# Performance work log

Hardware: AMD Instinct MI355X
Metric: run time of the kernel (lower is better)

## Reference

```python
import math
import jax, jax.numpy as jnp
import numpy as np

B, S, D = 1, 2048, 4096
H, KV, Dh = 32, 8, 128          # query heads, kv heads, head dim
G = H // KV                      # GQA group size
THETA = 10000.0
FACTOR = 4.0
BETA_FAST, BETA_SLOW, ORIG_MAX = 32, 1, 32768


def _yarn_rope_cache(seq_len):
    """YaRN-scaled RoPE cos/sin cache, matching YaRNRotaryEmbedding._build_cache."""
    inv_freq = 1.0 / (THETA ** (np.arange(0, Dh, 2, dtype=np.float32) / Dh))
    low = ORIG_MAX / (2 * math.pi * BETA_SLOW)
    high = ORIG_MAX / (2 * math.pi * BETA_FAST)
    freq = 1.0 / inv_freq
    smooth = np.clip((freq - low) / (high - low), 0.0, 1.0)
    inv_freq = (1.0 - smooth) * inv_freq + smooth * (inv_freq / FACTOR)
    t = np.arange(seq_len, dtype=np.float32)
    freqs = np.outer(t, inv_freq)                 # [S, Dh/2]
    emb = np.concatenate([freqs, freqs], axis=-1) # [S, Dh]
    return np.cos(emb).astype(np.float32), np.sin(emb).astype(np.float32)


def _rotate_half(x):
    x1, x2 = jnp.split(x, 2, axis=-1)
    return jnp.concatenate([-x2, x1], axis=-1)


def setup_inputs() -> dict:
    key = jax.random.key(0)
    k0, k1, k2, k3, k4 = jax.random.split(key, 5)
    scale = 0.02
    hidden_states = jax.random.normal(k0, (B, S, D), jnp.float32)
    Wq = jax.random.normal(k1, (H * Dh, D), jnp.float32) * scale
    Wk = jax.random.normal(k2, (KV * Dh, D), jnp.float32) * scale
    Wv = jax.random.normal(k3, (KV * Dh, D), jnp.float32) * scale
    Wo = jax.random.normal(k4, (D, H * Dh), jnp.float32) * scale
    cos_np, sin_np = _yarn_rope_cache(S)
    return {"hidden_states": hidden_states, "Wq": Wq, "Wk": Wk, "Wv": Wv,
            "Wo": Wo, "cos": jnp.asarray(cos_np), "sin": jnp.asarray(sin_np)}


def reference(hidden_states, Wq, Wk, Wv, Wo, cos, sin):
    x = hidden_states
    b, s, _ = x.shape
    # QKV projections (Linear, no bias): y = x @ W.T
    q = jnp.einsum('bsd,ed->bse', x, Wq).reshape(b, s, H, Dh).transpose(0, 2, 1, 3)   # [B,H,S,Dh]
    k = jnp.einsum('bsd,ed->bse', x, Wk).reshape(b, s, KV, Dh).transpose(0, 2, 1, 3)  # [B,KV,S,Dh]
    v = jnp.einsum('bsd,ed->bse', x, Wv).reshape(b, s, KV, Dh).transpose(0, 2, 1, 3)  # [B,KV,S,Dh]
    # YaRN RoPE (cos/sin: [S,Dh], broadcast over batch/head)
    c = cos[None, None, :, :]
    sn = sin[None, None, :, :]
    q = q * c + _rotate_half(q) * sn
    k = k * c + _rotate_half(k) * sn
    # GQA: group query heads over kv heads instead of materializing repeat_interleave
    qg = q.reshape(b, KV, G, s, Dh)
    scores = jnp.einsum('bkgqd,bknd->bkgqn', qg, k) / math.sqrt(Dh)  # [B,KV,G,S,S]
    causal = jnp.tril(jnp.ones((s, s), dtype=bool))
    scores = jnp.where(causal[None, None, None], scores, jnp.finfo(scores.dtype).min)
    w = jax.nn.softmax(scores.astype(jnp.float32), axis=-1).astype(x.dtype)
    attn = jnp.einsum('bkgqn,bknd->bkgqd', w, v)                      # [B,KV,G,S,Dh]
    attn = attn.reshape(b, H, s, Dh).transpose(0, 2, 1, 3).reshape(b, s, H * Dh)
    return jnp.einsum('bse,de->bsd', attn, Wo)
```

## Files before the change

### kernel.cpp

```cpp
#include <hip/hip_runtime.h>

#define S_LEN 2048
#define DMODEL 4096
#define NH 32
#define NKV 8
#define DH 128
#define QDIM (NH*DH)
#define NQKV 6144
#define SCALE 0.08838834764831845f

typedef __attribute__((ext_vector_type(8))) short short8;
typedef __attribute__((ext_vector_type(4))) float f32x4;
typedef __attribute__((ext_vector_type(4))) unsigned short us4;

__device__ __forceinline__ unsigned short f2bf(float f) {
  union { float f; unsigned int u; } v; v.f = f;
  unsigned int r = v.u + 0x7FFFu + ((v.u >> 16) & 1u);
  return (unsigned short)(r >> 16);
}
__device__ __forceinline__ float bf2f(unsigned short h) {
  union { unsigned int u; float f; } v; v.u = ((unsigned int)h) << 16;
  return v.f;
}
__device__ __forceinline__ short8 pack_bf16x8(float4 a, float4 b) {
  unsigned int u0, u1, u2, u3;
  asm("v_cvt_pk_bf16_f32 %0, %1, %2" : "=v"(u0) : "v"(a.x), "v"(a.y));
  asm("v_cvt_pk_bf16_f32 %0, %1, %2" : "=v"(u1) : "v"(a.z), "v"(a.w));
  asm("v_cvt_pk_bf16_f32 %0, %1, %2" : "=v"(u2) : "v"(b.x), "v"(b.y));
  asm("v_cvt_pk_bf16_f32 %0, %1, %2" : "=v"(u3) : "v"(b.z), "v"(b.w));
  union { unsigned int u[4]; short8 s; } r;
  r.u[0] = u0; r.u[1] = u1; r.u[2] = u2; r.u[3] = u3;
  return r.s;
}

__global__ __launch_bounds__(256) void cvt_x(const float* __restrict__ in,
                                             unsigned short* __restrict__ out) {
  int i = blockIdx.x * 256 + threadIdx.x;
  const float4 f = reinterpret_cast<const float4*>(in)[i];
  us4 o;
  o.x = f2bf(f.x); o.y = f2bf(f.y); o.z = f2bf(f.z); o.w = f2bf(f.w);
  reinterpret_cast<us4*>(out)[i] = o;
}

__global__ __launch_bounds__(512) void gemm8pqkv(const unsigned short* __restrict__ A,
                                                 const float* __restrict__ Wq,
                                                 const float* __restrict__ Wk,
                                                 const float* __restrict__ Wv,
                                                 unsigned short* __restrict__ Cv) {
  constexpr int K_ = 4096, N_ = 6144;
  constexpr int BM_ = 256, BN_ = 192;
  constexpr int ATILE = BM_ * 128;
  constexpr int BTILE = BN_ * 128;
  constexpr int BUF = ATILE + BTILE;
  constexpr int LPA = BM_ / 64;
  constexpr int LPB = BN_ / 64;
  constexpr int MI = 8, NF = 3;
  constexpr int MIL = 4, NFL = 1;
  constexpr int NT = K_ / 64;
  constexpr int CHN = 4;
  __shared__ char lds[2 * BUF];

  const int tid = threadIdx.x;
  const int lane = tid & 63, wave = tid >> 6;
  const int wm = wave >> 2, wn = wave & 3;
  const int fr = lane & 15, fq = lane >> 4;

  const int lin = blockIdx.x;
  const int xcd = lin & 7;
  const int slot = lin >> 3;
  const long n0 = (long)(xcd * CHN + slot % CHN) * BN_;
  const long m0 = (long)(slot / CHN) * BM_;

  const char* pB[LPB];
  int bslot[LPB];
#pragma unroll
  for (int u = 0; u < LPB; ++u) {
    int b = u * 8192 + tid * 16;
    int row = b >> 7;
    int colx = (b & 127) ^ ((row & 7) << 4);
    long n = n0 + row;
    const float* base = (n < 4096) ? Wq + n * (long)K_
                      : (n < 5120) ? Wk + (n - 4096) * (long)K_
                                   : Wv + (n - 5120) * (long)K_;
    pB[u] = (const char*)base + (long)colx * 2;
    bslot[u] = b;
  }
  float4 breg[LPB][2];

  auto B_ISSUE = [&](int t) {
#pragma unroll
    for (int u = 0; u < LPB; ++u) {
      breg[u][0] = *reinterpret_cast<const float4*>(pB[u] + (long)t * 256);
      breg[u][1] = *reinterpret_cast<const float4*>(pB[u] + (long)t * 256 + 16);
    }
  };
  auto B_WRITE = [&](int c) {
#pragma unroll
    for (int u = 0; u < LPB; ++u)
      *reinterpret_cast<short8*>(lds + c * BUF + ATILE + bslot[u]) =
          pack_bf16x8(breg[u][0], breg[u][1]);
  };
  auto STAGE_A = [&](int t, int c) {
#pragma unroll
    for (int u = 0; u < LPA; ++u) {
      int b = u * 8192 + tid * 16;
      int row = b >> 7;
      int off = (b & 127) ^ ((row & 7) << 4);
      __builtin_amdgcn_global_load_lds(
        (const __attribute__((address_space(1))) void*)((const char*)A + ((m0 + row) * (long)K_ + t * 64) * 2 + off),
        (__attribute__((address_space(3))) void*)(lds + c * BUF + b), 16, 0, 0);
    }
  };

  f32x4 acc[MI][NF] = {};
  short8 af[MI][2];
  short8 bf[NF][2];

  B_ISSUE(0);
  asm volatile("s_waitcnt vmcnt(0)" ::: "memory");
  B_WRITE(0);
  B_ISSUE(1);
  STAGE_A(0, 0); STAGE_A(1, 1);
  asm volatile("s_waitcnt vmcnt(8)" ::: "memory");
  B_WRITE(1);
  asm volatile("s_waitcnt vmcnt(0)" ::: "memory");
  asm volatile("s_waitcnt lgkmcnt(0)" ::: "memory");
  __builtin_amdgcn_s_barrier();

  for (int t = 0; t < NT; ++t) {
    const int c = t & 1;
    const char* tb = lds + c * BUF;

#pragma unroll
    for (int mi = 0; mi < MIL; ++mi) {
      int row = wm * (BM_ / 2) + mi * 16 + fr;
#pragma unroll
      for (int ks = 0; ks < 2; ++ks)
        af[mi][ks] = *(const short8*)(tb + row * 128 + ((ks * 64 + fq * 16) ^ ((row & 7) << 4)));
    }
#pragma unroll
    for (int ni = 0; ni < NFL; ++ni) {
      int row = wn * (BN_ / 4) + ni * 16 + fr;
#pragma unroll
      for (int ks = 0; ks < 2; ++ks)
        bf[ni][ks] = *(const short8*)(tb + ATILE + row * 128 + ((ks * 64 + fq * 16) ^ ((row & 7) << 4)));
    }
    asm volatile("s_waitcnt vmcnt(4)" ::: "memory");
    if (t > 0 && t + 1 < NT) B_WRITE((t + 1) & 1);
    if (t + 2 < NT) B_ISSUE(t + 2);
    __builtin_amdgcn_s_barrier();
    __builtin_amdgcn_s_setprio(1);
#pragma unroll
    for (int mi = 0; mi < MIL; ++mi)
#pragma unroll
      for (int ni = 0; ni < NFL; ++ni)
#pragma unroll
        for (int ks = 0; ks < 2; ++ks)
          acc[mi][ni] = __builtin_amdgcn_mfma_f32_16x16x32_bf16(af[mi][ks], bf[ni][ks], acc[mi][ni], 0, 0, 0);
    __builtin_amdgcn_s_setprio(0);
    __builtin_amdgcn_s_barrier();

#pragma unroll
    for (int mi = MIL; mi < MI; ++mi) {
      int row = wm * (BM_ / 2) + mi * 16 + fr;
#pragma unroll
      for (int ks = 0; ks < 2; ++ks)
        af[mi][ks] = *(const short8*)(tb + row * 128 + ((ks * 64 + fq * 16) ^ ((row & 7) << 4)));
    }
#pragma unroll
    for (int ni = NFL; ni < NF; ++ni) {
      int row = wn * (BN_ / 4) + ni * 16 + fr;
#pragma unroll
      for (int ks = 0; ks < 2; ++ks)
        bf[ni][ks] = *(const short8*)(tb + ATILE + row * 128 + ((ks * 64 + fq * 16) ^ ((row & 7) << 4)));
    }
    __builtin_amdgcn_s_barrier();
    __builtin_amdgcn_s_setprio(1);
#pragma unroll
    for (int mi = 0; mi < MIL; ++mi)
#pragma unroll
      for (int ni = NFL; ni < NF; ++ni)
#pragma unroll
        for (int ks = 0; ks < 2; ++ks)
          acc[mi][ni] = __builtin_amdgcn_mfma_f32_16x16x32_bf16(af[mi][ks], bf[ni][ks], acc[mi][ni], 0, 0, 0);
    __builtin_amdgcn_s_setprio(0);
    __builtin_amdgcn_s_barrier();

    if (t + 2 < NT) STAGE_A(t + 2, c);
    __builtin_amdgcn_s_setprio(1);
#pragma unroll
    for (int mi = MIL; mi < MI; ++mi)
#pragma unroll
      for (int ni = 0; ni < NFL; ++ni)
#pragma unroll
        for (int ks = 0; ks < 2; ++ks)
          acc[mi][ni] = __builtin_amdgcn_mfma_f32_16x16x32_bf16(af[mi][ks], bf[ni][ks], acc[mi][ni], 0, 0, 0);
    __builtin_amdgcn_s_setprio(0);
    __builtin_amdgcn_s_barrier();

    __builtin_amdgcn_s_setprio(1);
#pragma unroll
    for (int mi = MIL; mi < MI; ++mi)
#pragma unroll
      for (int ni = NFL; ni < NF; ++ni)
#pragma unroll
        for (int ks = 0; ks < 2; ++ks)
          acc[mi][ni] = __builtin_amdgcn_mfma_f32_16x16x32_bf16(af[mi][ks], bf[ni][ks], acc[mi][ni], 0, 0, 0);
    __builtin_amdgcn_s_setprio(0);
    if (t + 2 < NT) { asm volatile("s_waitcnt vmcnt(10)" ::: "memory"); }
    else if (t + 1 < NT) { asm volatile("s_waitcnt vmcnt(0)" ::: "memory"); }
    __builtin_amdgcn_s_barrier();
  }

#pragma unroll
  for (int mi = 0; mi < MI; ++mi)
#pragma unroll
    for (int ni = 0; ni < NF; ++ni)
#pragma unroll
      for (int j = 0; j < 4; ++j) {
        long r = m0 + wm * (BM_ / 2) + mi * 16 + fq * 4 + j;
        long cc = n0 + wn * (BN_ / 4) + ni * 16 + fr;
        Cv[r * N_ + cc] = f2bf(acc[mi][ni][j]);
      }
}

template<int M_, int N_, int K_, int BM_, int BN_, int OUT_BF16, int CHN>
__global__ __launch_bounds__(512) void gemm8p(const unsigned short* __restrict__ A,
                                              const unsigned short* __restrict__ B,
                                              void* __restrict__ Cv) {
  constexpr int ATILE = BM_ * 128;
  constexpr int BTILE = BN_ * 128;
  constexpr int BUF = ATILE + BTILE;
  constexpr int LPA = BM_ / 64;
  constexpr int LPB = BN_ / 64;
  constexpr int VM  = LPA + LPB;
  constexpr int MI = BM_ / 32, NF = BN_ / 64;
  constexpr int MIL = MI / 2, NFL = NF / 2;
  constexpr int NT = K_ / 64;
  __shared__ char lds[2 * BUF];

  const int tid = threadIdx.x;
  const int lane = tid & 63, wave = tid >> 6;
  const int wm = wave >> 2, wn = wave & 3;
  const int fr = lane & 15, fq = lane >> 4;

  const int lin = blockIdx.x;
  const int xcd = lin & 7;
  const int slot = lin >> 3;
  const long n0 = (long)(xcd * CHN + slot % CHN) * BN_;
  const long m0 = (long)(slot / CHN) * BM_;

  auto STAGE_A = [&](int t, int c) {
#pragma unroll
    for (int u = 0; u < LPA; ++u) {
      int b = u * 8192 + tid * 16;
      int row = b >> 7;
      int off = (b & 127) ^ ((row & 7) << 4);
      __builtin_amdgcn_global_load_lds(
        (const __attribute__((address_space(1))) void*)((const char*)A + ((m0 + row) * (long)K_ + t * 64) * 2 + off),
        (__attribute__((address_space(3))) void*)(lds + c * BUF + b), 16, 0, 0);
    }
  };
  auto STAGE_B = [&](int t, int c) {
#pragma unroll
    for (int u = 0; u < LPB; ++u) {
      int b = u * 8192 + tid * 16;
      int row = b >> 7;
      int off = (b & 127) ^ ((row & 7) << 4);
      __builtin_amdgcn_global_load_lds(
        (const __attribute__((address_space(1))) void*)((const char*)B + ((n0 + row) * (long)K_ + t * 64) * 2 + off),
        (__attribute__((address_space(3))) void*)(lds + c * BUF + ATILE + b), 16, 0, 0);
    }
  };
#define VMCNT_STEADY() do { if constexpr (VM == 6) asm volatile("s_waitcnt vmcnt(6)" ::: "memory"); \
                            else if constexpr (VM == 7) asm volatile("s_waitcnt vmcnt(7)" ::: "memory"); \
                            else asm volatile("s_waitcnt vmcnt(8)" ::: "memory"); } while (0)

  f32x4 acc[MI][NF] = {};
  short8 af[MI][2];
  short8 bf[NF][2];

  STAGE_A(0, 0); STAGE_B(0, 0);
  STAGE_A(1, 1); STAGE_B(1, 1);
  VMCNT_STEADY();
  __builtin_amdgcn_s_barrier();

  for (int t = 0; t < NT; ++t) {
    const int c = t & 1;
    const char* tb = lds + c * BUF;

#pragma unroll
    for (int mi = 0; mi < MIL; ++mi) {
      int row = wm * (BM_ / 2) + mi * 16 + fr;
#pragma unroll
      for (int ks = 0; ks < 2; ++ks)
        af[mi][ks] = *(const short8*)(tb + row * 128 + ((ks * 64 + fq * 16) ^ ((row & 7) << 4)));
    }
#pragma unroll
    for (int ni = 0; ni < NFL; ++ni) {
      int row = wn * (BN_ / 4) + ni * 16 + fr;
#pragma unroll
      for (int ks = 0; ks < 2; ++ks)
        bf[ni][ks] = *(const short8*)(tb + ATILE + row * 128 + ((ks * 64 + fq * 16) ^ ((row & 7) << 4)));
    }
    __builtin_amdgcn_s_barrier();
    __builtin_amdgcn_s_setprio(1);
#pragma unroll
    for (int mi = 0; mi < MIL; ++mi)
#pragma unroll
      for (int ni = 0; ni < NFL; ++ni)
#pragma unroll
        for (int ks = 0; ks < 2; ++ks)
          acc[mi][ni] = __builtin_amdgcn_mfma_f32_16x16x32_bf16(af[mi][ks], bf[ni][ks], acc[mi][ni], 0, 0, 0);
    __builtin_amdgcn_s_setprio(0);
    __builtin_amdgcn_s_barrier();

#pragma unroll
    for (int mi = MIL; mi < MI; ++mi) {
      int row = wm * (BM_ / 2) + mi * 16 + fr;
#pragma unroll
      for (int ks = 0; ks < 2; ++ks)
        af[mi][ks] = *(const short8*)(tb + row * 128 + ((ks * 64 + fq * 16) ^ ((row & 7) << 4)));
    }
#pragma unroll
    for (int ni = NFL; ni < NF; ++ni) {
      int row = wn * (BN_ / 4) + ni * 16 + fr;
#pragma unroll
      for (int ks = 0; ks < 2; ++ks)
        bf[ni][ks] = *(const short8*)(tb + ATILE + row * 128 + ((ks * 64 + fq * 16) ^ ((row & 7) << 4)));
    }
    __builtin_amdgcn_s_barrier();
    __builtin_amdgcn_s_setprio(1);
#pragma unroll
    for (int mi = 0; mi < MIL; ++mi)
#pragma unroll
      for (int ni = NFL; ni < NF; ++ni)
#pragma unroll
        for (int ks = 0; ks < 2; ++ks)
          acc[mi][ni] = __builtin_amdgcn_mfma_f32_16x16x32_bf16(af[mi][ks], bf[ni][ks], acc[mi][ni], 0, 0, 0);
    __builtin_amdgcn_s_setprio(0);
    __builtin_amdgcn_s_barrier();

    if (t + 2 < NT) STAGE_A(t + 2, c);
    __builtin_amdgcn_s_setprio(1);
#pragma unroll
    for (int mi = MIL; mi < MI; ++mi)
#pragma unroll
      for (int ni = 0; ni < NFL; ++ni)
#pragma unroll
        for (int ks = 0; ks < 2; ++ks)
          acc[mi][ni] = __builtin_amdgcn_mfma_f32_16x16x32_bf16(af[mi][ks], bf[ni][ks], acc[mi][ni], 0, 0, 0);
    __builtin_amdgcn_s_setprio(0);
    __builtin_amdgcn_s_barrier();

    if (t + 2 < NT) STAGE_B(t + 2, c);
    __builtin_amdgcn_s_setprio(1);
#pragma unroll
    for (int mi = MIL; mi < MI; ++mi)
#pragma unroll
      for (int ni = NFL; ni < NF; ++ni)
#pragma unroll
        for (int ks = 0; ks < 2; ++ks)
          acc[mi][ni] = __builtin_amdgcn_mfma_f32_16x16x32_bf16(af[mi][ks], bf[ni][ks], acc[mi][ni], 0, 0, 0);
    __builtin_amdgcn_s_setprio(0);
    if (t + 2 < NT) { VMCNT_STEADY(); }
    else if (t + 1 < NT) { asm volatile("s_waitcnt vmcnt(0)" ::: "memory"); }
    __builtin_amdgcn_s_barrier();
  }
#undef VMCNT_STEADY

#pragma unroll
  for (int mi = 0; mi < MI; ++mi)
#pragma unroll
    for (int ni = 0; ni < NF; ++ni)
#pragma unroll
      for (int j = 0; j < 4; ++j) {
        long r = m0 + wm * (BM_ / 2) + mi * 16 + fq * 4 + j;
        long cc = n0 + wn * (BN_ / 4) + ni * 16 + fr;
        float v = acc[mi][ni][j];
        if (OUT_BF16) ((unsigned short*)Cv)[r * N_ + cc] = f2bf(v);
        else          ((float*)Cv)[r * N_ + cc] = v;
      }
}

__global__ __launch_bounds__(256) void ropek_tv(unsigned short* __restrict__ C,
                                                const float* __restrict__ cosb,
                                                const float* __restrict__ sinb,
                                                unsigned short* __restrict__ VT) {
  __shared__ unsigned short tbuf[64][72];
  const int blk = blockIdx.x;
  if (blk < 4096) {
    int idx = blk * 256 + threadIdx.x;
    int i = idx & 63;
    int t = idx >> 6;
    int hh = t & 7;
    int s = t >> 3;
    unsigned short* row = C + (size_t)s * NQKV + 4096 + hh * DH;
    float c  = cosb[s * DH + i];
    float sn = sinb[s * DH + i];
    float x1 = bf2f(row[i]);
    float x2 = bf2f(row[i + 64]);
    row[i]      = f2bf(x1 * c - x2 * sn);
    row[i + 64] = f2bf(x2 * c + x1 * sn);
    return;
  }
  const int b2 = blk - 4096;
  const unsigned short* Vbuf = C + 5120;
  const int s0 = (b2 & 31) * 64, e0 = (b2 >> 5) * 64;
  const int r = threadIdx.x >> 3, c = (threadIdx.x & 7) * 8;
#pragma unroll
  for (int half = 0; half < 2; ++half) {
    int row = r + half * 32;
    *reinterpret_cast<short8*>(&tbuf[row][c]) =
        *reinterpret_cast<const short8*>(Vbuf + (size_t)(s0 + row) * NQKV + e0 + c);
  }
  __syncthreads();
  const int hh = e0 >> 7, dbase = e0 & 127;
#pragma unroll
  for (int half = 0; half < 2; ++half) {
    int row = r + half * 32;
    short8 o;
#pragma unroll
    for (int j = 0; j < 8; ++j) ((unsigned short*)&o)[j] = tbuf[c + j][row];
    *reinterpret_cast<short8*>(VT + (size_t)hh * (DH * (size_t)S_LEN)
                               + (size_t)(dbase + row) * S_LEN + s0 + c) = o;
  }
}

__global__ __launch_bounds__(256) void attn_fwd(const unsigned short* __restrict__ C,
                                                const unsigned short* __restrict__ VT,
                                                unsigned short* __restrict__ Ob,
                                                const float* __restrict__ Wo,
                                                unsigned short* __restrict__ Wob,
                                                const float* __restrict__ cosb,
                                                const float* __restrict__ sinb) {
  __shared__ unsigned short KVs[2][8192];
  __shared__ unsigned short Pl[4][16 * 40];
  const int tid = threadIdx.x, lane = tid & 63, wave = tid >> 6;
  const int kvh = blockIdx.x & 7;
  const int p = blockIdx.x >> 3;
  const int h = kvh * 4 + wave;
  const int fr = lane & 15, fq = lane >> 4;
  const int q0s[2] = { p * 16, (127 - p) * 16 };
  const int tilesA = (p * 16 + 47) >> 5;
  const int tilesB = ((127 - p) * 16 + 47) >> 5;

  const unsigned short* Qbase = C + (size_t)h * DH;
  const unsigned short* Kbase = C + 4096 + (size_t)kvh * DH;
  const unsigned short* Vbase = VT + (size_t)kvh * (DH * (size_t)S_LEN);

  const int wq0 = blockIdx.x * 8192 + tid;
  float4 wreg;

  short8 qf[2][4];
#pragma unroll
  for (int s = 0; s < 2; ++s)
#pragma unroll
    for (int dc = 0; dc < 4; ++dc)
      qf[s][dc] = *reinterpret_cast<const short8*>(
          Qbase + (size_t)(q0s[s] + fr) * NQKV + dc * 32 + fq * 8);

#pragma unroll
  for (int s = 0; s < 2; ++s) {
    const int row = q0s[s] + fr;
#pragma unroll
    for (int dc = 0; dc < 2; ++dc)
#pragma unroll
      for (int e = 0; e < 8; ++e) {
        int d = dc * 32 + fq * 8 + e;
        float cs = cosb[row * DH + d];
        float sn = sinb[row * DH + d];
        float x1 = bf2f((unsigned short)qf[s][dc][e]);
        float x2 = bf2f((unsigned short)qf[s][dc + 2][e]);
        qf[s][dc][e]     = (short)f2bf((x1 * cs - x2 * sn) * SCALE);
        qf[s][dc + 2][e] = (short)f2bf((x2 * cs + x1 * sn) * SCALE);
      }
  }

  f32x4 o_acc[2][8] = {};
  float mrow[2][4] = {{-1e30f,-1e30f,-1e30f,-1e30f},{-1e30f,-1e30f,-1e30f,-1e30f}};
  float lpart[2][4] = {};

  auto STAGE = [&](int t, int buf) {
    const int kv0 = t * 32;
    char* dst = (char*)&KVs[buf][0];
#pragma unroll
    for (int sh = 0; sh < 2; ++sh) {
      int b = sh * 4096 + tid * 16;
      int krow = b >> 8;
      int kcol = (b & 255) ^ ((krow & 7) << 4);
      __builtin_amdgcn_global_load_lds(
          (const __attribute__((address_space(1))) void*)(Kbase + (size_t)(kv0 + krow) * NQKV + (kcol >> 1)),
          (__attribute__((address_space(3))) void*)(dst + b), 16, 0, 0);
      int vrow = b >> 6;
      int vcol = (b & 63) ^ ((((vrow ^ (vrow >> 2)) & 3)) << 4);
      __builtin_amdgcn_global_load_lds(
          (const __attribute__((address_space(1))) void*)(Vbase + (size_t)vrow * S_LEN + kv0 + (vcol >> 1)),
          (__attribute__((address_space(3))) void*)(dst + 8192 + b), 16, 0, 0);
    }
  };

  int cur = 0;
  STAGE(0, 0);
  asm volatile("s_waitcnt vmcnt(0)" ::: "memory");
  __syncthreads();

  for (int t = 0; t < tilesB; ++t) {
    const int kv0 = t * 32;

    if (t > 0 && t <= 32) {
      us4 o;
      o.x = f2bf(wreg.x); o.y = f2bf(wreg.y); o.z = f2bf(wreg.z); o.w = f2bf(wreg.w);
      reinterpret_cast<us4*>(Wob)[wq0 + (t - 1) * 256] = o;
    }
    if (t < 32) wreg = reinterpret_cast<const float4*>(Wo)[wq0 + t * 256];

    if (t + 1 < tilesB) STAGE(t + 1, cur ^ 1);
    const char* kvb = (const char*)&KVs[cur][0];

#pragma unroll
    for (int s = 0; s < 2; ++s) {
      if (s == 0 && t >= tilesA) continue;
      const int q0 = q0s[s];

      f32x4 sacc[2] = {};
#pragma unroll
      for (int nt = 0; nt < 2; ++nt) {
        const int row = nt * 16 + fr;
#pragma unroll
        for (int dc = 0; dc < 4; ++dc) {
          short8 kf = *reinterpret_cast<const short8*>(
              kvb + row * 256 + ((dc * 64 + fq * 16) ^ ((row & 7) << 4)));
          sacc[nt] = __builtin_amdgcn_mfma_f32_16x16x32_bf16(qf[s][dc], kf, sacc[nt], 0, 0, 0);
        }
      }

      const bool needMask = (kv0 + 32 > q0);
      if (needMask) {
#pragma unroll
        for (int j = 0; j < 4; ++j) {
          int qrow = q0 + fq * 4 + j;
#pragma unroll
          for (int nt = 0; nt < 2; ++nt)
            sacc[nt][j] = ((kv0 + nt*16 + fr) <= qrow) ? sacc[nt][j] : -1e30f;
        }
      }
      bool ok = true;
      float lm[4];
#pragma unroll
      for (int j = 0; j < 4; ++j) {
        lm[j] = fmaxf(sacc[0][j], sacc[1][j]);
        ok = ok && (lm[j] <= mrow[s][j] + 8.f);
      }
      if (!__all(ok)) {
#pragma unroll
        for (int j = 0; j < 4; ++j) {
          float rm = lm[j];
          rm = fmaxf(rm, __shfl_xor(rm, 1));
          rm = fmaxf(rm, __shfl_xor(rm, 2));
          rm = fmaxf(rm, __shfl_xor(rm, 4));
          rm = fmaxf(rm, __shfl_xor(rm, 8));
          float mnew = fmaxf(mrow[s][j], rm);
          float corr = __expf(mrow[s][j] - mnew);
          mrow[s][j] = mnew;
          lpart[s][j] *= corr;
#pragma unroll
          for (int dt = 0; dt < 8; ++dt) o_acc[s][dt][j] *= corr;
        }
      }
#pragma unroll
      for (int j = 0; j < 4; ++j) {
        float p0 = __expf(sacc[0][j] - mrow[s][j]);
        float p1 = __expf(sacc[1][j] - mrow[s][j]);
        lpart[s][j] += p0 + p1;
        unsigned int u;
        asm("v_cvt_pk_bf16_f32 %0, %1, %2" : "=v"(u) : "v"(p0), "v"(p1));
        Pl[wave][(fq*4 + j)*40 + fr]      = (unsigned short)u;
        Pl[wave][(fq*4 + j)*40 + 16 + fr] = (unsigned short)(u >> 16);
      }
      asm volatile("s_waitcnt lgkmcnt(0)" ::: "memory");
      __builtin_amdgcn_sched_barrier(0);

      short8 pa = *reinterpret_cast<const short8*>(&Pl[wave][fr*40 + fq*8]);
#pragma unroll
      for (int dt = 0; dt < 8; ++dt) {
        const int row = dt * 16 + fr;
        short8 bv = *reinterpret_cast<const short8*>(
            kvb + 8192 + row * 64 + ((fq * 16) ^ ((((row ^ (row >> 2)) & 3)) << 4)));
        o_acc[s][dt] = __builtin_amdgcn_mfma_f32_16x16x32_bf16(pa, bv, o_acc[s][dt], 0, 0, 0);
      }
    }

    asm volatile("s_waitcnt vmcnt(0)" ::: "memory");
    __syncthreads();
    cur ^= 1;
  }

#pragma unroll
  for (int s = 0; s < 2; ++s)
#pragma unroll
    for (int j = 0; j < 4; ++j) {
      float l = lpart[s][j];
      l += __shfl_xor(l, 1);
      l += __shfl_xor(l, 2);
      l += __shfl_xor(l, 4);
      l += __shfl_xor(l, 8);
      float inv = 1.f / l;
      size_t r = (size_t)q0s[s] + fq*4 + j;
#pragma unroll
      for (int dt = 0; dt < 8; ++dt)
        Ob[r * QDIM + h * DH + dt*16 + fr] = f2bf(o_acc[s][dt][j] * inv);
    }
}

extern "C" void kernel_launch(void* const* d_in, const int* in_sizes, int n_in,
                              void* d_out, int out_size, void* d_ws, size_t ws_size,
                              hipStream_t stream) {
  (void)in_sizes; (void)n_in; (void)out_size; (void)ws_size;
  const float* x    = (const float*)d_in[0];
  const float* Wq   = (const float*)d_in[1];
  const float* Wk   = (const float*)d_in[2];
  const float* Wv   = (const float*)d_in[3];
  const float* Wo   = (const float*)d_in[4];
  const float* cosb = (const float*)d_in[5];
  const float* sinb = (const float*)d_in[6];

  char* ws = (char*)d_ws;
  unsigned short* xb    = (unsigned short*)(ws);
  unsigned short* Wob   = (unsigned short*)(ws + 67108864);
  unsigned short* Cqkv  = (unsigned short*)(ws + 100663296);
  unsigned short* VT    = (unsigned short*)(ws + 125829120);
  unsigned short* Ab    = xb;

  cvt_x<<<8192, 256, 0, stream>>>(x, xb);

  gemm8pqkv<<<256, 512, 0, stream>>>(xb, Wq, Wk, Wv, Cqkv);

  ropek_tv<<<4608, 256, 0, stream>>>(Cqkv, cosb, sinb, VT);

  attn_fwd<<<512, 256, 0, stream>>>(Cqkv, VT, Ab, Wo, Wob, cosb, sinb);

  gemm8p<2048, 4096, 4096, 128, 256, 0, 2><<<256, 512, 0, stream>>>(Ab, Wob, d_out);
}
```

Measured before the change: 285.3 us.

## Double-buffer weight prefetch registers and unroll QKV GEMM K-loop by two

Splits the fp32 weight prefetch registers into two alternating sets and unrolls the K-loop by two, so each tile's global loads go into the set not currently waiting to be converted. The bf16 conversion and LDS write of the next B tile move later in the iteration, after the A-stage issue, with retuned vmcnt waits. The aim is to hide weight-load latency behind more MFMA work. The cost is more VGPRs, which could hurt occupancy or cause spills. The first-quadrant MFMA code is also hard-coded to a single B fragment, which assumes NFL is 1.

```diff
diff --git a/kernel.cpp b/kernel.cpp
--- a/kernel.cpp
+++ b/kernel.cpp
@@ -85,21 +85,21 @@
     pB[u] = (const char*)base + (long)colx * 2;
     bslot[u] = b;
   }
-  float4 breg[LPB][2];
-
-  auto B_ISSUE = [&](int t) {
-#pragma unroll
-    for (int u = 0; u < LPB; ++u) {
-      breg[u][0] = *reinterpret_cast<const float4*>(pB[u] + (long)t * 256);
-      breg[u][1] = *reinterpret_cast<const float4*>(pB[u] + (long)t * 256 + 16);
-    }
-  };
-  auto B_WRITE = [&](int c) {
-#pragma unroll
-    for (int u = 0; u < LPB; ++u)
-      *reinterpret_cast<short8*>(lds + c * BUF + ATILE + bslot[u]) =
-          pack_bf16x8(breg[u][0], breg[u][1]);
-  };
+  float4 bregs0[LPB][2], bregs1[LPB][2];
+
+#define B_ISSUE(T, REGS) do { \
+  _Pragma("unroll") \
+  for (int u = 0; u < LPB; ++u) { \
+    REGS[u][0] = *reinterpret_cast<const float4*>(pB[u] + (long)(T) * 256); \
+    REGS[u][1] = *reinterpret_cast<const float4*>(pB[u] + (long)(T) * 256 + 16); \
+  } } while (0)
+#define B_WRITE(C, REGS) do { \
+  _Pragma("unroll") \
+  for (int u = 0; u < LPB; ++u) \
+    *reinterpret_cast<short8*>(lds + (C) * BUF + ATILE + bslot[u]) = \
+        pack_bf16x8(REGS[u][0], REGS[u][1]); \
+  } while (0)
+
   auto STAGE_A = [&](int t, int c) {
 #pragma unroll
     for (int u = 0; u < LPA; ++u) {
@@ -116,101 +116,105 @@
   short8 af[MI][2];
   short8 bf[NF][2];
 
-  B_ISSUE(0);
+  B_ISSUE(0, bregs0);
   asm volatile("s_waitcnt vmcnt(0)" ::: "memory");
-  B_WRITE(0);
-  B_ISSUE(1);
+  B_WRITE(0, bregs0);
+  B_ISSUE(1, bregs1);
   STAGE_A(0, 0); STAGE_A(1, 1);
-  asm volatile("s_waitcnt vmcnt(8)" ::: "memory");
-  B_WRITE(1);
-  asm volatile("s_waitcnt vmcnt(0)" ::: "memory");
+  asm volatile("s_waitcnt vmcnt(4)" ::: "memory");
   asm volatile("s_waitcnt lgkmcnt(0)" ::: "memory");
   __builtin_amdgcn_s_barrier();
 
-  for (int t = 0; t < NT; ++t) {
-    const int c = t & 1;
-    const char* tb = lds + c * BUF;
-
-#pragma unroll
-    for (int mi = 0; mi < MIL; ++mi) {
-      int row = wm * (BM_ / 2) + mi * 16 + fr;
-#pragma unroll
-      for (int ks = 0; ks < 2; ++ks)
-        af[mi][ks] = *(const short8*)(tb + row * 128 + ((ks * 64 + fq * 16) ^ ((row & 7) << 4)));
-    }
-#pragma unroll
-    for (int ni = 0; ni < NFL; ++ni) {
-      int row = wn * (BN_ / 4) + ni * 16 + fr;
-#pragma unroll
-      for (int ks = 0; ks < 2; ++ks)
-        bf[ni][ks] = *(const short8*)(tb + ATILE + row * 128 + ((ks * 64 + fq * 16) ^ ((row & 7) << 4)));
-    }
-    asm volatile("s_waitcnt vmcnt(4)" ::: "memory");
-    if (t > 0 && t + 1 < NT) B_WRITE((t + 1) & 1);
-    if (t + 2 < NT) B_ISSUE(t + 2);
-    __builtin_amdgcn_s_barrier();
-    __builtin_amdgcn_s_setprio(1);
-#pragma unroll
-    for (int mi = 0; mi < MIL; ++mi)
-#pragma unroll
-      for (int ni = 0; ni < NFL; ++ni)
-#pragma unroll
-        for (int ks = 0; ks < 2; ++ks)
-          acc[mi][ni] = __builtin_amdgcn_mfma_f32_16x16x32_bf16(af[mi][ks], bf[ni][ks], acc[mi][ni], 0, 0, 0);
-    __builtin_amdgcn_s_setprio(0);
-    __builtin_amdgcn_s_barrier();
-
-#pragma unroll
-    for (int mi = MIL; mi < MI; ++mi) {
-      int row = wm * (BM_ / 2) + mi * 16 + fr;
-#pragma unroll
-      for (int ks = 0; ks < 2; ++ks)
-        af[mi][ks] = *(const short8*)(tb + row * 128 + ((ks * 64 + fq * 16) ^ ((row & 7) << 4)));
-    }
-#pragma unroll
-    for (int ni = NFL; ni < NF; ++ni) {
-      int row = wn * (BN_ / 4) + ni * 16 + fr;
-#pragma unroll
-      for (int ks = 0; ks < 2; ++ks)
-        bf[ni][ks] = *(const short8*)(tb + ATILE + row * 128 + ((ks * 64 + fq * 16) ^ ((row & 7) << 4)));
-    }
-    __builtin_amdgcn_s_barrier();
-    __builtin_amdgcn_s_setprio(1);
-#pragma unroll
-    for (int mi = 0; mi < MIL; ++mi)
-#pragma unroll
-      for (int ni = NFL; ni < NF; ++ni)
-#pragma unroll
-        for (int ks = 0; ks < 2; ++ks)
-          acc[mi][ni] = __builtin_amdgcn_mfma_f32_16x16x32_bf16(af[mi][ks], bf[ni][ks], acc[mi][ni], 0, 0, 0);
-    __builtin_amdgcn_s_setprio(0);
-    __builtin_amdgcn_s_barrier();
-
-    if (t + 2 < NT) STAGE_A(t + 2, c);
-    __builtin_amdgcn_s_setprio(1);
-#pragma unroll
-    for (int mi = MIL; mi < MI; ++mi)
-#pragma unroll
-      for (int ni = 0; ni < NFL; ++ni)
-#pragma unroll
-        for (int ks = 0; ks < 2; ++ks)
-          acc[mi][ni] = __builtin_amdgcn_mfma_f32_16x16x32_bf16(af[mi][ks], bf[ni][ks], acc[mi][ni], 0, 0, 0);
-    __builtin_amdgcn_s_setprio(0);
-    __builtin_amdgcn_s_barrier();
-
-    __builtin_amdgcn_s_setprio(1);
-#pragma unroll
-    for (int mi = MIL; mi < MI; ++mi)
-#pragma unroll
-      for (int ni = NFL; ni < NF; ++ni)
-#pragma unroll
-        for (int ks = 0; ks < 2; ++ks)
-          acc[mi][ni] = __builtin_amdgcn_mfma_f32_16x16x32_bf16(af[mi][ks], bf[ni][ks], acc[mi][ni], 0, 0, 0);
-    __builtin_amdgcn_s_setprio(0);
-    if (t + 2 < NT) { asm volatile("s_waitcnt vmcnt(10)" ::: "memory"); }
-    else if (t + 1 < NT) { asm volatile("s_waitcnt vmcnt(0)" ::: "memory"); }
-    __builtin_amdgcn_s_barrier();
-  }
+#define KTILE(T, C, REGS_CUR, REGS_OTH) do { \
+  const int t_ = (T); \
+  const char* tb = lds + (C) * BUF; \
+   \
+  _Pragma("unroll") \
+  for (int mi = 0; mi < MIL; ++mi) { \
+    int row = wm * (BM_ / 2) + mi * 16 + fr; \
+    _Pragma("unroll") \
+    for (int ks = 0; ks < 2; ++ks) \
+      af[mi][ks] = *(const short8*)(tb + row * 128 + ((ks * 64 + fq * 16) ^ ((row & 7) << 4))); \
+  } \
+  { int row = wn * (BN_ / 4) + fr; \
+    _Pragma("unroll") \
+    for (int ks = 0; ks < 2; ++ks) \
+      bf[0][ks] = *(const short8*)(tb + ATILE + row * 128 + ((ks * 64 + fq * 16) ^ ((row & 7) << 4))); } \
+  if (t_ + 2 < NT) B_ISSUE(t_ + 2, REGS_CUR); \
+  __builtin_amdgcn_s_barrier(); \
+  __builtin_amdgcn_s_setprio(1); \
+  _Pragma("unroll") \
+  for (int mi = 0; mi < MIL; ++mi) \
+    _Pragma("unroll") \
+    for (int ks = 0; ks < 2; ++ks) \
+      acc[mi][0] = __builtin_amdgcn_mfma_f32_16x16x32_bf16(af[mi][ks], bf[0][ks], acc[mi][0], 0, 0, 0); \
+  __builtin_amdgcn_s_setprio(0); \
+  __builtin_amdgcn_s_barrier(); \
+   \
+  _Pragma("unroll") \
+  for (int mi = MIL; mi < MI; ++mi) { \
+    int row = wm * (BM_ / 2) + mi * 16 + fr; \
+    _Pragma("unroll") \
+    for (int ks = 0; ks < 2; ++ks) \
+      af[mi][ks] = *(const short8*)(tb + row * 128 + ((ks * 64 + fq * 16) ^ ((row & 7) << 4))); \
+  } \
+  _Pragma("unroll") \
+  for (int ni = NFL; ni < NF; ++ni) { \
+    int row = wn * (BN_ / 4) + ni * 16 + fr; \
+    _Pragma("unroll") \
+    for (int ks = 0; ks < 2; ++ks) \
+      bf[ni][ks] = *(const short8*)(tb + ATILE + row * 128 + ((ks * 64 + fq * 16) ^ ((row & 7) << 4))); \
+  } \
+  __builtin_amdgcn_s_barrier(); \
+  __builtin_amdgcn_s_setprio(1); \
+  _Pragma("unroll") \
+  for (int mi = 0; mi < MIL; ++mi) \
+    _Pragma("unroll") \
+    for (int ni = NFL; ni < NF; ++ni) \
+      _Pragma("unroll") \
+      for (int ks = 0; ks < 2; ++ks) \
+        acc[mi][ni] = __builtin_amdgcn_mfma_f32_16x16x32_bf16(af[mi][ks], bf[ni][ks], acc[mi][ni], 0, 0, 0); \
+  __builtin_amdgcn_s_setprio(0); \
+  __builtin_amdgcn_s_barrier(); \
+   \
+  if (t_ + 2 < NT) { \
+    STAGE_A(t_ + 2, (C)); \
+    asm volatile("s_waitcnt vmcnt(14)" ::: "memory"); \
+  } else { \
+    asm volatile("s_waitcnt vmcnt(0)" ::: "memory"); \
+  } \
+  if (t_ + 1 < NT) B_WRITE((C) ^ 1, REGS_OTH); \
+  __builtin_amdgcn_s_setprio(1); \
+  _Pragma("unroll") \
+  for (int mi = MIL; mi < MI; ++mi) \
+    _Pragma("unroll") \
+    for (int ks = 0; ks < 2; ++ks) \
+      acc[mi][0] = __builtin_amdgcn_mfma_f32_16x16x32_bf16(af[mi][ks], bf[0][ks], acc[mi][0], 0, 0, 0); \
+  __builtin_amdgcn_s_setprio(0); \
+  __builtin_amdgcn_s_barrier(); \
+   \
+  __builtin_amdgcn_s_setprio(1); \
+  _Pragma("unroll") \
+  for (int mi = MIL; mi < MI; ++mi) \
+    _Pragma("unroll") \
+    for (int ni = NFL; ni < NF; ++ni) \
+      _Pragma("unroll") \
+      for (int ks = 0; ks < 2; ++ks) \
+        acc[mi][ni] = __builtin_amdgcn_mfma_f32_16x16x32_bf16(af[mi][ks], bf[ni][ks], acc[mi][ni], 0, 0, 0); \
+  __builtin_amdgcn_s_setprio(0); \
+  if (t_ + 2 < NT) { asm volatile("s_waitcnt vmcnt(10)" ::: "memory"); } \
+  else if (t_ + 1 < NT) { asm volatile("s_waitcnt vmcnt(0)" ::: "memory"); } \
+  asm volatile("s_waitcnt lgkmcnt(0)" ::: "memory"); \
+  __builtin_amdgcn_s_barrier(); \
+} while (0)
+
+  for (int it = 0; it < NT / 2; ++it) {
+    KTILE(2 * it,     0, bregs0, bregs1);
+    KTILE(2 * it + 1, 1, bregs1, bregs0);
+  }
+#undef KTILE
+#undef B_ISSUE
+#undef B_WRITE
 
 #pragma unroll
   for (int mi = 0; mi < MI; ++mi)
```

Measured after the change: 419.9 us. 1.47x slower.
